# Kernel tuning notes

Measured on AMD Instinct MI355X. Metric: run time of the kernel, lower is better.

Reference implementation:

```python
import jax, jax.numpy as jnp
import numpy as np


def setup_inputs() -> dict:
    key = jax.random.key(0)
    ks = jax.random.split(key, 6)
    b, t, k, h = 2, 2048, 256, 8
    s = 1.0 / np.sqrt(k)
    return {
        "x": jax.random.normal(ks[0], (b, t, k), dtype=jnp.float32),
        "Wq": jax.random.normal(ks[1], (k, k * h), dtype=jnp.float32) * s,
        "Wk": jax.random.normal(ks[2], (k, k * h), dtype=jnp.float32) * s,
        "Wv": jax.random.normal(ks[3], (k, k * h), dtype=jnp.float32) * s,
        "Wu": jax.random.normal(ks[4], (k * h, k), dtype=jnp.float32) * (1.0 / np.sqrt(k * h)),
        "bu": jnp.zeros((k,), dtype=jnp.float32),
    }


def reference(x, Wq, Wk, Wv, Wu, bu):
    b, t, k = x.shape
    h = Wq.shape[1] // k
    scale = k ** (-0.25)
    # projections -> [b, t, h, k] -> [b, h, t, k]
    q = (x @ Wq).reshape(b, t, h, k).transpose(0, 2, 1, 3) * scale
    kk = (x @ Wk).reshape(b, t, h, k).transpose(0, 2, 1, 3) * scale
    v = (x @ Wv).reshape(b, t, h, k).transpose(0, 2, 1, 3)
    dot = jnp.einsum('bhqk,bhsk->bhqs', q, kk)  # [b,h,t,t]
    attn = jax.nn.softmax(dot, axis=-1)
    out = jnp.einsum('bhqs,bhsk->bhqk', attn, v)  # [b,h,t,k]
    out = out.transpose(0, 2, 1, 3).reshape(b, t, h * k)
    return out @ Wu + bu
```

## Files before the change

kernel.cpp:

```cpp
#include <hip/hip_runtime.h>

using bf16x8   = __bf16 __attribute__((ext_vector_type(8)));
using floatx4  = float __attribute__((ext_vector_type(4)));
using floatx16 = float __attribute__((ext_vector_type(16)));

static __device__ __forceinline__ unsigned short f2b(float x) {
  unsigned u = __builtin_bit_cast(unsigned, x);
  u = (u + 0x7fffu + ((u >> 16) & 1u)) >> 16;
  return (unsigned short)u;
}

static __device__ __forceinline__ void gl_lds16(const unsigned short* g, unsigned short* l) {
  __builtin_amdgcn_global_load_lds((const __attribute__((address_space(1))) void*)g,
                                   (__attribute__((address_space(3))) void*)l, 16, 0, 0);
}

__global__ __launch_bounds__(256) void prep_kernel(const float* __restrict__ x,
                                                   const float* __restrict__ Wq,
                                                   const float* __restrict__ Wk,
                                                   const float* __restrict__ Wv,
                                                   const float* __restrict__ Wu,
                                                   unsigned short* __restrict__ xb,
                                                   unsigned short* __restrict__ wqkt,
                                                   unsigned short* __restrict__ wvt,
                                                   unsigned short* __restrict__ wut) {
  int bx = blockIdx.x;
  if (bx < 1024) {
    int i = (bx * 256 + threadIdx.x) * 4;
    float4 v = *(const float4*)(x + i);
    unsigned long long p = (unsigned long long)f2b(v.x) |
                           ((unsigned long long)f2b(v.y) << 16) |
                           ((unsigned long long)f2b(v.z) << 32) |
                           ((unsigned long long)f2b(v.w) << 48);
    *(unsigned long long*)(xb + i) = p;
    return;
  }
  __shared__ unsigned short T[64][65];
  const float* src;
  unsigned short* dst;
  int R, C, tile;
  if (bx < 1152)      { src = Wq; dst = wqkt;          R = 256;  C = 2048; tile = bx - 1024; }
  else if (bx < 1280) { src = Wk; dst = wqkt + 524288; R = 256;  C = 2048; tile = bx - 1152; }
  else if (bx < 1408) { src = Wv; dst = wvt;           R = 256;  C = 2048; tile = bx - 1280; }
  else                { src = Wu; dst = wut;           R = 2048; C = 256;  tile = bx - 1408; }
  int ctiles = C >> 6;
  int cx = tile % ctiles, ry = tile / ctiles;
  int r0 = ry * 64, c0 = cx * 64;
  int t = threadIdx.x;
#pragma unroll
  for (int i = 0; i < 16; ++i) {
    int idx = i * 256 + t;
    int r = idx >> 6, c = idx & 63;
    T[r][c] = f2b(src[(size_t)(r0 + r) * C + c0 + c]);
  }
  __syncthreads();
#pragma unroll
  for (int i = 0; i < 16; ++i) {
    int idx = i * 256 + t;
    int c = idx >> 6, r = idx & 63;
    dst[(size_t)(c0 + c) * R + r0 + r] = T[r][c];
  }
}

__global__ __launch_bounds__(256) void proj_kernel(const unsigned short* __restrict__ A,
                                                   const unsigned short* __restrict__ Bt,
                                                   unsigned short* __restrict__ qkb,
                                                   unsigned short* __restrict__ vtb) {
  __shared__ unsigned short As[128 * 32];
  __shared__ unsigned short Bs[128 * 32];
  const int Kt = 256;
  int tid = threadIdx.x, lane = tid & 63, w = tid >> 6;
  int m16 = lane & 15, quad = lane >> 4;
  int wr = w & 1, wc = w >> 1;
  int m0 = blockIdx.y * 128, n0 = blockIdx.x * 128;
  int srow0 = w * 32 + (lane >> 2);
  int schunk = (lane & 3) ^ ((lane >> 2) & 3);
  floatx4 acc[4][4] = {};
  for (int k0 = 0; k0 < Kt; k0 += 32) {
    __syncthreads();
#pragma unroll
    for (int j = 0; j < 2; ++j) {
      int r = srow0 + j * 16;
      gl_lds16(A + (size_t)(m0 + r) * Kt + k0 + schunk * 8, &As[(w * 32 + j * 16) * 32]);
      gl_lds16(Bt + (size_t)(n0 + r) * Kt + k0 + schunk * 8, &Bs[(w * 32 + j * 16) * 32]);
    }
    __syncthreads();
    int sw = (quad ^ (m16 & 3)) * 8;
    bf16x8 af[4], bfr[4];
#pragma unroll
    for (int i = 0; i < 4; ++i) {
      af[i]  = *(const bf16x8*)(&As[(wr * 64 + i * 16 + m16) * 32 + sw]);
      bfr[i] = *(const bf16x8*)(&Bs[(wc * 64 + i * 16 + m16) * 32 + sw]);
    }
#pragma unroll
    for (int i = 0; i < 4; ++i)
#pragma unroll
      for (int jn = 0; jn < 4; ++jn)
        acc[i][jn] = __builtin_amdgcn_mfma_f32_16x16x32_bf16(af[i], bfr[jn], acc[i][jn], 0, 0, 0);
  }
  if (n0 < 4096) {
#pragma unroll
    for (int i = 0; i < 4; ++i)
#pragma unroll
      for (int jn = 0; jn < 4; ++jn)
#pragma unroll
        for (int r = 0; r < 4; ++r) {
          int m = m0 + wr * 64 + i * 16 + quad * 4 + r;
          int n = n0 + wc * 64 + jn * 16 + m16;
          qkb[(size_t)m * 4096 + n] = f2b(acc[i][jn][r]);
        }
  } else {
#pragma unroll
    for (int i = 0; i < 4; ++i)
#pragma unroll
      for (int jn = 0; jn < 4; ++jn)
#pragma unroll
        for (int r = 0; r < 4; ++r) {
          int m = m0 + wr * 64 + i * 16 + quad * 4 + r;
          int nn = n0 - 4096 + wc * 64 + jn * 16 + m16;
          int bb = m >> 11, t = m & 2047;
          vtb[((size_t)(bb * 2048 + nn)) * 2048 + t] = f2b(acc[i][jn][r]);
        }
  }
}

__global__ __launch_bounds__(256) void out_kernel(const unsigned short* __restrict__ A,
                                                  const unsigned short* __restrict__ Bt,
                                                  float* __restrict__ Cout,
                                                  const float* __restrict__ bias) {
  __shared__ unsigned short As[64 * 64];
  __shared__ unsigned short Bs[64 * 64];
  const int Kt = 2048;
  int tid = threadIdx.x, lane = tid & 63, w = tid >> 6;
  int m16 = lane & 15, quad = lane >> 4;
  int m0 = blockIdx.y * 64, n0 = blockIdx.x * 64;
  int srow_i = lane >> 3;
  int schunk = (lane & 7) ^ srow_i;
  int rsw = m16 & 7;
  floatx4 acc[4] = {};
  for (int k0 = 0; k0 < Kt; k0 += 64) {
    __syncthreads();
#pragma unroll
    for (int j = 0; j < 2; ++j) {
      int r = w * 16 + j * 8 + srow_i;
      gl_lds16(A + (size_t)(m0 + r) * Kt + k0 + schunk * 8, &As[(w * 16 + j * 8) * 64]);
      gl_lds16(Bt + (size_t)(n0 + r) * Kt + k0 + schunk * 8, &Bs[(w * 16 + j * 8) * 64]);
    }
    __syncthreads();
    bf16x8 af[2];
#pragma unroll
    for (int kk = 0; kk < 2; ++kk)
      af[kk] = *(const bf16x8*)(&As[(w * 16 + m16) * 64 + (((kk * 4 + quad) ^ rsw) * 8)]);
#pragma unroll
    for (int nt = 0; nt < 4; ++nt)
#pragma unroll
      for (int kk = 0; kk < 2; ++kk) {
        bf16x8 bfv = *(const bf16x8*)(&Bs[(nt * 16 + m16) * 64 + (((kk * 4 + quad) ^ rsw) * 8)]);
        acc[nt] = __builtin_amdgcn_mfma_f32_16x16x32_bf16(af[kk], bfv, acc[nt], 0, 0, 0);
      }
  }
#pragma unroll
  for (int nt = 0; nt < 4; ++nt)
#pragma unroll
    for (int r = 0; r < 4; ++r) {
      int m = m0 + w * 16 + quad * 4 + r;
      int n = n0 + nt * 16 + m16;
      Cout[(size_t)m * 256 + n] = acc[nt][r] + bias[n];
    }
}

__global__ __launch_bounds__(256, 2) void attn_kernel(const unsigned short* __restrict__ qk,
                                                      const unsigned short* __restrict__ vt,
                                                      unsigned short* __restrict__ ao) {
  __shared__ unsigned short Ks[64 * 256];
  __shared__ unsigned short Vs[256 * 64];
  __shared__ unsigned short Pb[2][32 * 72];
  int tid = threadIdx.x, lane = tid & 63, w = tid >> 6;
  int c32 = lane & 31, hi = lane >> 5;
  int qh = w & 1, u = w >> 1;
  int id = blockIdx.x;
  int xcd = id & 7, j = id >> 3;
  int bh = xcd + 8 * (j & 1);
  int q0 = (j >> 1) * 64;
  int b = bh >> 3, h = bh & 7;

  bf16x8 qf[16];
  const unsigned short* qrow =
      qk + (size_t)(b * 2048 + q0 + qh * 32 + c32) * 4096 + h * 256 + hi * 8;
#pragma unroll
  for (int kk = 0; kk < 16; ++kk) qf[kk] = *(const bf16x8*)(qrow + kk * 16);

  bf16x8 onesf;
#pragma unroll
  for (int i = 0; i < 8; ++i) onesf[i] = (__bf16)1.0f;

  floatx16 O[4] = {};
  floatx16 l = {};

  const unsigned short* kbase = qk + (size_t)b * 2048 * 4096 + 2048 + h * 256;
  const unsigned short* vbase = vt + (size_t)bh * 256 * 2048;
  unsigned short* pq = &Pb[qh][0];

  int krow_i = lane >> 5, kpos = lane & 31;
  int vrow_i = lane >> 3, vpos = lane & 7;
  int ksw = c32 & 7;

  for (int st = 0; st < 32; ++st) {
    int s0 = st * 64;
    __syncthreads();
#pragma unroll
    for (int i = 0; i < 8; ++i) {
      int kr = i * 2 + krow_i;
      gl_lds16(kbase + (size_t)(s0 + w * 16 + kr) * 4096 + ((kpos ^ (kr & 7)) * 8),
               &Ks[(w * 16 + i * 2) * 256]);
      gl_lds16(vbase + (size_t)(w * 64 + i * 8 + vrow_i) * 2048 + s0 + ((vpos ^ vrow_i) * 8),
               &Vs[(w * 64 + i * 8) * 64]);
    }
    __syncthreads();

    floatx16 s = {};
    const unsigned short* krl = &Ks[(u * 32 + c32) * 256];
#pragma unroll
    for (int kk = 0; kk < 16; ++kk) {
      bf16x8 kf = *(const bf16x8*)(krl + (((kk * 2 + hi) ^ ksw) * 8));
      s = __builtin_amdgcn_mfma_f32_32x32x16_bf16(qf[kk], kf, s, 0, 0, 0);
    }
#pragma unroll
    for (int i = 0; i < 16; ++i) {
      float p = __expf(s[i] * 0.0625f);
      int q = (i & 3) + 8 * (i >> 2) + 4 * hi;
      pq[q * 72 + u * 32 + c32] = f2b(p);
    }
    __syncthreads();

    bf16x8 paf[4];
#pragma unroll
    for (int f = 0; f < 4; ++f) paf[f] = *(const bf16x8*)(pq + c32 * 72 + f * 16 + hi * 8);
#pragma unroll
    for (int f = 0; f < 4; ++f)
      l = __builtin_amdgcn_mfma_f32_32x32x16_bf16(paf[f], onesf, l, 0, 0, 0);
#pragma unroll
    for (int dt = 0; dt < 4; ++dt) {
      const unsigned short* vrl = &Vs[(u * 128 + dt * 32 + c32) * 64];
#pragma unroll
      for (int f = 0; f < 4; ++f) {
        bf16x8 vf = *(const bf16x8*)(vrl + (((f * 2 + hi) ^ ksw) * 8));
        O[dt] = __builtin_amdgcn_mfma_f32_32x32x16_bf16(paf[f], vf, O[dt], 0, 0, 0);
      }
    }
  }
  float inv[16];
#pragma unroll
  for (int i = 0; i < 16; ++i) inv[i] = 1.0f / l[i];
#pragma unroll
  for (int dt = 0; dt < 4; ++dt)
#pragma unroll
    for (int i = 0; i < 16; ++i) {
      int q = (i & 3) + 8 * (i >> 2) + 4 * hi;
      ao[(size_t)(b * 2048 + q0 + qh * 32 + q) * 2048 + h * 256 + u * 128 + dt * 32 + c32] =
          f2b(O[dt][i] * inv[i]);
    }
}

extern "C" void kernel_launch(void* const* d_in, const int* in_sizes, int n_in,
                              void* d_out, int out_size, void* d_ws, size_t ws_size,
                              hipStream_t stream) {
  const float* x  = (const float*)d_in[0];
  const float* Wq = (const float*)d_in[1];
  const float* Wk = (const float*)d_in[2];
  const float* Wv = (const float*)d_in[3];
  const float* Wu = (const float*)d_in[4];
  const float* bu = (const float*)d_in[5];

  unsigned short* xb   = (unsigned short*)d_ws;
  unsigned short* wqkt = xb + 1048576;
  unsigned short* wvt  = wqkt + 1048576;
  unsigned short* wut  = wvt + 524288;
  unsigned short* qkb  = wut + 524288;
  unsigned short* vtb  = qkb + 16777216;
  unsigned short* aob  = vtb + 8388608;

  prep_kernel<<<1536, 256, 0, stream>>>(x, Wq, Wk, Wv, Wu, xb, wqkt, wvt, wut);
  proj_kernel<<<dim3(48, 32), 256, 0, stream>>>(xb, wqkt, qkb, vtb);
  attn_kernel<<<512, 256, 0, stream>>>(qkb, vtb, aob);
  out_kernel<<<dim3(4, 64), 256, 0, stream>>>(aob, wut, (float*)d_out, bu);
}
```

Baseline: 213.2 us.

## Double-buffer K/V tiles in attention, widen blocks, stage V transpose via LDS

The attention kernel now uses 512 threads covering 128 queries per block and double-buffers the K and V tiles in LDS. The next tile's global-to-LDS loads are issued before the PV matmul, so memory latency can overlap compute. The projection kernel stages the V-transpose output through shared memory to make coalesced 16-byte stores in place of scattered 2-byte writes. LDS use per attention block roughly doubles (about 146KB), which may cap it at one block per CU and leaves only 256 blocks to fill the GPU.

New measurement: 200.9 us. -5.8%, faster.

```diff
diff --git a/kernel.cpp b/kernel.cpp
--- a/kernel.cpp
+++ b/kernel.cpp
@@ -66,8 +66,9 @@
                                                    const unsigned short* __restrict__ Bt,
                                                    unsigned short* __restrict__ qkb,
                                                    unsigned short* __restrict__ vtb) {
-  __shared__ unsigned short As[128 * 32];
-  __shared__ unsigned short Bs[128 * 32];
+  __shared__ __align__(16) unsigned short SMEM[128 * 136];
+  unsigned short* As = SMEM;
+  unsigned short* Bs = SMEM + 4096;
   const int Kt = 256;
   int tid = threadIdx.x, lane = tid & 63, w = tid >> 6;
   int m16 = lane & 15, quad = lane >> 4;
@@ -110,17 +111,28 @@
           qkb[(size_t)m * 4096 + n] = f2b(acc[i][jn][r]);
         }
   } else {
+    __syncthreads();
+    unsigned short* Vt = SMEM;
 #pragma unroll
     for (int i = 0; i < 4; ++i)
 #pragma unroll
       for (int jn = 0; jn < 4; ++jn)
 #pragma unroll
         for (int r = 0; r < 4; ++r) {
-          int m = m0 + wr * 64 + i * 16 + quad * 4 + r;
-          int nn = n0 - 4096 + wc * 64 + jn * 16 + m16;
-          int bb = m >> 11, t = m & 2047;
-          vtb[((size_t)(bb * 2048 + nn)) * 2048 + t] = f2b(acc[i][jn][r]);
+          int nn = wc * 64 + jn * 16 + m16;
+          int mm = wr * 64 + i * 16 + quad * 4 + r;
+          Vt[nn * 136 + mm] = f2b(acc[i][jn][r]);
         }
+    __syncthreads();
+    int bb = m0 >> 11, t0 = m0 & 2047;
+#pragma unroll
+    for (int i2 = 0; i2 < 8; ++i2) {
+      int idx = i2 * 256 + tid;
+      int nn = idx >> 4;
+      int mc = (idx & 15) * 8;
+      uint4 v = *(const uint4*)(&Vt[nn * 136 + mc]);
+      *(uint4*)(&vtb[((size_t)(bb * 2048 + n0 - 4096 + nn)) * 2048 + t0 + mc]) = v;
+    }
   }
 }
 
@@ -169,24 +181,24 @@
     }
 }
 
-__global__ __launch_bounds__(256, 2) void attn_kernel(const unsigned short* __restrict__ qk,
+__global__ __launch_bounds__(512, 2) void attn_kernel(const unsigned short* __restrict__ qk,
                                                       const unsigned short* __restrict__ vt,
                                                       unsigned short* __restrict__ ao) {
-  __shared__ unsigned short Ks[64 * 256];
-  __shared__ unsigned short Vs[256 * 64];
-  __shared__ unsigned short Pb[2][32 * 72];
+  __shared__ __align__(16) unsigned short Ks[2][64 * 256];
+  __shared__ __align__(16) unsigned short Vs[2][256 * 64];
+  __shared__ __align__(16) unsigned short Pb[4][32 * 72];
   int tid = threadIdx.x, lane = tid & 63, w = tid >> 6;
   int c32 = lane & 31, hi = lane >> 5;
-  int qh = w & 1, u = w >> 1;
+  int qg = w & 3, u = w >> 2;
   int id = blockIdx.x;
   int xcd = id & 7, j = id >> 3;
   int bh = xcd + 8 * (j & 1);
-  int q0 = (j >> 1) * 64;
+  int q0 = (j >> 1) * 128;
   int b = bh >> 3, h = bh & 7;
 
   bf16x8 qf[16];
   const unsigned short* qrow =
-      qk + (size_t)(b * 2048 + q0 + qh * 32 + c32) * 4096 + h * 256 + hi * 8;
+      qk + (size_t)(b * 2048 + q0 + qg * 32 + c32) * 4096 + h * 256 + hi * 8;
 #pragma unroll
   for (int kk = 0; kk < 16; ++kk) qf[kk] = *(const bf16x8*)(qrow + kk * 16);
 
@@ -199,27 +211,28 @@
 
   const unsigned short* kbase = qk + (size_t)b * 2048 * 4096 + 2048 + h * 256;
   const unsigned short* vbase = vt + (size_t)bh * 256 * 2048;
-  unsigned short* pq = &Pb[qh][0];
+  unsigned short* pq = &Pb[qg][0];
 
   int krow_i = lane >> 5, kpos = lane & 31;
   int vrow_i = lane >> 3, vpos = lane & 7;
   int ksw = c32 & 7;
 
+#pragma unroll
+  for (int i = 0; i < 4; ++i) {
+    int kr = i * 2 + krow_i;
+    gl_lds16(kbase + (size_t)(w * 8 + kr) * 4096 + ((kpos ^ (kr & 7)) * 8),
+             &Ks[0][(w * 8 + i * 2) * 256]);
+    int vr = i * 8 + vrow_i;
+    gl_lds16(vbase + (size_t)(w * 32 + vr) * 2048 + ((vpos ^ vrow_i) * 8),
+             &Vs[0][(w * 32 + i * 8) * 64]);
+  }
+
   for (int st = 0; st < 32; ++st) {
-    int s0 = st * 64;
-    __syncthreads();
-#pragma unroll
-    for (int i = 0; i < 8; ++i) {
-      int kr = i * 2 + krow_i;
-      gl_lds16(kbase + (size_t)(s0 + w * 16 + kr) * 4096 + ((kpos ^ (kr & 7)) * 8),
-               &Ks[(w * 16 + i * 2) * 256]);
-      gl_lds16(vbase + (size_t)(w * 64 + i * 8 + vrow_i) * 2048 + s0 + ((vpos ^ vrow_i) * 8),
-               &Vs[(w * 64 + i * 8) * 64]);
-    }
+    int cur = st & 1;
     __syncthreads();
 
     floatx16 s = {};
-    const unsigned short* krl = &Ks[(u * 32 + c32) * 256];
+    const unsigned short* krl = &Ks[cur][(u * 32 + c32) * 256];
 #pragma unroll
     for (int kk = 0; kk < 16; ++kk) {
       bf16x8 kf = *(const bf16x8*)(krl + (((kk * 2 + hi) ^ ksw) * 8));
@@ -233,6 +246,21 @@
     }
     __syncthreads();
 
+    if (st < 31) {
+      int s0 = (st + 1) * 64;
+      unsigned short* kdst = &Ks[1 - cur][0];
+      unsigned short* vdst = &Vs[1 - cur][0];
+#pragma unroll
+      for (int i = 0; i < 4; ++i) {
+        int kr = i * 2 + krow_i;
+        gl_lds16(kbase + (size_t)(s0 + w * 8 + kr) * 4096 + ((kpos ^ (kr & 7)) * 8),
+                 kdst + (w * 8 + i * 2) * 256);
+        int vr = i * 8 + vrow_i;
+        gl_lds16(vbase + (size_t)(w * 32 + vr) * 2048 + s0 + ((vpos ^ vrow_i) * 8),
+                 vdst + (w * 32 + i * 8) * 64);
+      }
+    }
+
     bf16x8 paf[4];
 #pragma unroll
     for (int f = 0; f < 4; ++f) paf[f] = *(const bf16x8*)(pq + c32 * 72 + f * 16 + hi * 8);
@@ -241,7 +269,7 @@
       l = __builtin_amdgcn_mfma_f32_32x32x16_bf16(paf[f], onesf, l, 0, 0, 0);
 #pragma unroll
     for (int dt = 0; dt < 4; ++dt) {
-      const unsigned short* vrl = &Vs[(u * 128 + dt * 32 + c32) * 64];
+      const unsigned short* vrl = &Vs[cur][(u * 128 + dt * 32 + c32) * 64];
 #pragma unroll
       for (int f = 0; f < 4; ++f) {
         bf16x8 vf = *(const bf16x8*)(vrl + (((f * 2 + hi) ^ ksw) * 8));
@@ -257,7 +285,7 @@
 #pragma unroll
     for (int i = 0; i < 16; ++i) {
       int q = (i & 3) + 8 * (i >> 2) + 4 * hi;
-      ao[(size_t)(b * 2048 + q0 + qh * 32 + q) * 2048 + h * 256 + u * 128 + dt * 32 + c32] =
+      ao[(size_t)(b * 2048 + q0 + qg * 32 + q) * 2048 + h * 256 + u * 128 + dt * 32 + c32] =
           f2b(O[dt][i] * inv[i]);
     }
 }
@@ -282,6 +310,6 @@
 
   prep_kernel<<<1536, 256, 0, stream>>>(x, Wq, Wk, Wv, Wu, xb, wqkt, wvt, wut);
   proj_kernel<<<dim3(48, 32), 256, 0, stream>>>(xb, wqkt, qkb, vtb);
-  attn_kernel<<<512, 256, 0, stream>>>(qkb, vtb, aob);
+  attn_kernel<<<256, 512, 0, stream>>>(qkb, vtb, aob);
   out_kernel<<<dim3(4, 64), 256, 0, stream>>>(aob, wut, (float*)d_out, bu);
 }
```
